# Optimization experiments

Measured on AMD Instinct MI355X. Metric: run time of the kernel, lower is better.

Reference implementation:

```python
import jax, jax.numpy as jnp
import numpy as np

HIDDEN = 4096
NUM_HEADS = 32
NUM_KV_HEADS = 8
HEAD_DIM = 128
EPS = 1e-6
ROPE_THETA = 1000000.0
T = 2048


def setup_inputs() -> dict:
    key = jax.random.key(0)
    k1, k2, k3, k4, k5 = jax.random.split(key, 5)
    q_size = NUM_HEADS * HEAD_DIM
    kv_size = NUM_KV_HEADS * HEAD_DIM
    return {
        "positions": jnp.arange(T, dtype=jnp.int32),
        "hidden_states": jax.random.normal(k1, (T, HIDDEN), dtype=jnp.float32),
        "w_qkv": jax.random.normal(k2, (HIDDEN, q_size + 2 * kv_size), dtype=jnp.float32) * 0.02,
        "w_o": jax.random.normal(k3, (q_size, HIDDEN), dtype=jnp.float32) * 0.02,
        "q_norm_w": jnp.ones((HEAD_DIM,), dtype=jnp.float32) + 0.01 * jax.random.normal(k4, (HEAD_DIM,), dtype=jnp.float32),
        "k_norm_w": jnp.ones((HEAD_DIM,), dtype=jnp.float32) + 0.01 * jax.random.normal(k5, (HEAD_DIM,), dtype=jnp.float32),
    }


def _rms_norm(x, w, eps=EPS):
    # x: [..., head_dim], normalize over last dim
    var = jnp.mean(jnp.square(x), axis=-1, keepdims=True)
    return x * jax.lax.rsqrt(var + eps) * w


def _apply_rope(x, positions):
    # neox-style rotate-half RoPE, rotary_dim == head_dim
    d = x.shape[-1]
    inv_freq = 1.0 / (ROPE_THETA ** (jnp.arange(0, d, 2, dtype=jnp.float32) / d))
    freqs = positions.astype(jnp.float32)[:, None] * inv_freq[None, :]  # [T, d/2]
    cos = jnp.cos(freqs)[:, None, :]  # [T, 1, d/2]
    sin = jnp.sin(freqs)[:, None, :]
    x1, x2 = jnp.split(x, 2, axis=-1)
    return jnp.concatenate([x1 * cos - x2 * sin, x2 * cos + x1 * sin], axis=-1)


def reference(positions, hidden_states, w_qkv, w_o, q_norm_w, k_norm_w):
    num_tokens = hidden_states.shape[0]
    q_size = NUM_HEADS * HEAD_DIM
    kv_size = NUM_KV_HEADS * HEAD_DIM
    group = NUM_HEADS // NUM_KV_HEADS

    qkv = hidden_states @ w_qkv  # [T, q+2kv]
    q = qkv[:, :q_size].reshape(num_tokens, NUM_HEADS, HEAD_DIM)
    k = qkv[:, q_size:q_size + kv_size].reshape(num_tokens, NUM_KV_HEADS, HEAD_DIM)
    v = qkv[:, q_size + kv_size:].reshape(num_tokens, NUM_KV_HEADS, HEAD_DIM)

    q = _rms_norm(q, q_norm_w)
    k = _rms_norm(k, k_norm_w)
    q = _apply_rope(q, positions)
    k = _apply_rope(k, positions)

    scale = HEAD_DIM ** -0.5
    # GQA: group query heads over shared kv heads
    qg = q.reshape(num_tokens, NUM_KV_HEADS, group, HEAD_DIM)
    scores = jnp.einsum("tkgd,skd->kgts", qg * scale, k)  # [KH, G, T, S]
    causal = positions[:, None] >= positions[None, :]  # [T, S]
    scores = jnp.where(causal[None, None, :, :], scores, jnp.finfo(scores.dtype).min)
    probs = jax.nn.softmax(scores, axis=-1)
    out = jnp.einsum("kgts,skd->tkgd", probs, v)  # [T, KH, G, D]
    out = out.reshape(num_tokens, q_size)
    return out @ w_o
```

## Files before the change

### kernel.cpp

```cpp
#include <hip/hip_runtime.h>
#include <cstdint>
#include <cstddef>

#define T_TOK 2048
#define HID   4096
#define NQH   32
#define NKVH  8
#define HD    128
#define QKV_N 6144

typedef __bf16 bf16x8 __attribute__((ext_vector_type(8)));
typedef __bf16 bf16x4 __attribute__((ext_vector_type(4)));
typedef float  f32x4  __attribute__((ext_vector_type(4)));
typedef float  f32x16 __attribute__((ext_vector_type(16)));

#define AS1 __attribute__((address_space(1)))
#define AS3 __attribute__((address_space(3)))

__device__ __forceinline__ void gll16(const void* g, void* l) {
  __builtin_amdgcn_global_load_lds((const AS1 void*)g, (AS3 void*)l, 16, 0, 0);
}

__global__ __launch_bounds__(256) void k_convert(const float* __restrict__ in,
                                                 __bf16* __restrict__ out, int n4) {
  int i = blockIdx.x * 256 + threadIdx.x;
  if (i >= n4) return;
  float4 v = ((const float4*)in)[i];
  bf16x4 o;
  o[0] = (__bf16)v.x; o[1] = (__bf16)v.y; o[2] = (__bf16)v.z; o[3] = (__bf16)v.w;
  ((bf16x4*)out)[i] = o;
}

__global__ __launch_bounds__(256) void k_transpose(const float* __restrict__ in,
                                                   __bf16* __restrict__ out,
                                                   int R, int C) {
  __shared__ float tile[64][65];
  const int tid = threadIdx.x;
  const int c0 = blockIdx.x * 64, r0 = blockIdx.y * 64;
  const int ty = tid >> 4, tx = tid & 15;
#pragma unroll
  for (int k = 0; k < 4; ++k) {
    float4 v = *(const float4*)&in[(size_t)(r0 + ty + k * 16) * C + c0 + tx * 4];
    tile[ty + k * 16][tx * 4 + 0] = v.x;
    tile[ty + k * 16][tx * 4 + 1] = v.y;
    tile[ty + k * 16][tx * 4 + 2] = v.z;
    tile[ty + k * 16][tx * 4 + 3] = v.w;
  }
  __syncthreads();
  const int c = tid >> 2, rq = tid & 3;
#pragma unroll
  for (int h = 0; h < 2; ++h) {
    bf16x8 o;
#pragma unroll
    for (int i = 0; i < 8; ++i) o[i] = (__bf16)tile[rq * 16 + h * 8 + i][c];
    *(bf16x8*)&out[(size_t)(c0 + c) * R + r0 + rq * 16 + h * 8] = o;
  }
}

template <int NFR, typename OUT>
__global__ __launch_bounds__(512, 2) void k_gemm8(const __bf16* __restrict__ A,
                                                  const __bf16* __restrict__ Bt,
                                                  OUT* __restrict__ C,
                                                  int N, int K) {
  constexpr int BN   = 64 * NFR;
  constexpr int WN   = 16 * NFR;
  constexpr int NB   = NFR / 2;
  constexpr int NH   = NFR / 2;
  constexpr int BREG = BN * 64;
  constexpr int BUFSZ = 16384 + 2 * BREG;
  __shared__ alignas(16) char ldsb[2 * BUFSZ];
  const int tid = threadIdx.x;
  const int lane = tid & 63, w = tid >> 6;
  const int l16 = lane & 15, lg = lane >> 4;
  const int wm = w >> 2, wn = w & 3;

  const int x = blockIdx.x & 7, idx = blockIdx.x >> 3;
  const int bm = (x & 1) * 8 + (idx & 7);
  const int bn = (x >> 1) * 4 + (idx >> 3);

  const int rA = tid >> 2, pA = tid & 3;
  const __bf16* asrc = A + (size_t)(bm * 128 + rA) * K + ((pA ^ ((rA >> 1) & 3)) * 8);
  const __bf16* bsrc = Bt + (size_t)(bn * BN + rA) * K + ((pA ^ ((rA >> 1) & 3)) * 8);

#define RA_(buf, mk) (ldsb + (buf) * BUFSZ + (mk) * 8192)
#define RB_(buf, mk) (ldsb + (buf) * BUFSZ + 16384 + (mk) * BREG)
#define STG_A(buf, mk, kk) { gll16(asrc + (kk) + (mk) * 32, RA_(buf, mk) + w * 1024); }
#define STG_B(buf, mk, kk) { _Pragma("unroll") \
    for (int j = 0; j < NB; ++j) \
      gll16(bsrc + (size_t)j * 128 * K + (kk) + (mk) * 32, RB_(buf, mk) + j * 8192 + w * 1024); }
#define FRAG(base, row) (*(const bf16x8*)((base) + (row) * 64 + ((lg ^ (((row) >> 1) & 3)) << 4)))
#define WAITN() { if constexpr (NFR == 6) asm volatile("s_waitcnt vmcnt(4)" ::: "memory"); \
                  else                    asm volatile("s_waitcnt vmcnt(3)" ::: "memory"); }

  f32x4 acc[4][NFR] = {};
  const int nkt = K >> 6;

  STG_A(0, 0, 0); STG_B(0, 0, 0); STG_A(0, 1, 0); STG_B(0, 1, 0);

  for (int t = 0; t < nkt - 1; ++t) {
    const int cur = t & 1, nxt = cur ^ 1;
    const int kn = (t + 1) * 64;
    bf16x8 af[4], bf_[NH];

    STG_A(nxt, 0, kn);
    WAITN();
    __builtin_amdgcn_s_barrier();
    __builtin_amdgcn_sched_barrier(0);
#pragma unroll
    for (int i = 0; i < 4; ++i) af[i] = FRAG(RA_(cur, 0), wm * 64 + i * 16 + l16);
#pragma unroll
    for (int n = 0; n < NH; ++n) bf_[n] = FRAG(RB_(cur, 0), wn * WN + n * 16 + l16);
    __builtin_amdgcn_s_setprio(1);
#pragma unroll
    for (int i = 0; i < 4; ++i)
#pragma unroll
      for (int n = 0; n < NH; ++n)
        acc[i][n] = __builtin_amdgcn_mfma_f32_16x16x32_bf16(af[i], bf_[n], acc[i][n], 0, 0, 0);
    __builtin_amdgcn_s_setprio(0);
    __builtin_amdgcn_s_barrier();

#pragma unroll
    for (int n = 0; n < NH; ++n) bf_[n] = FRAG(RB_(cur, 0), wn * WN + (NH + n) * 16 + l16);
    STG_B(nxt, 0, kn);
    __builtin_amdgcn_s_barrier();
    __builtin_amdgcn_s_setprio(1);
#pragma unroll
    for (int i = 0; i < 4; ++i)
#pragma unroll
      for (int n = 0; n < NH; ++n)
        acc[i][NH + n] = __builtin_amdgcn_mfma_f32_16x16x32_bf16(af[i], bf_[n], acc[i][NH + n], 0, 0, 0);
    __builtin_amdgcn_s_setprio(0);
    __builtin_amdgcn_s_barrier();

    STG_A(nxt, 1, kn);
    WAITN();
    __builtin_amdgcn_s_barrier();
    __builtin_amdgcn_sched_barrier(0);
#pragma unroll
    for (int i = 0; i < 4; ++i) af[i] = FRAG(RA_(cur, 1), wm * 64 + i * 16 + l16);
#pragma unroll
    for (int n = 0; n < NH; ++n) bf_[n] = FRAG(RB_(cur, 1), wn * WN + n * 16 + l16);
    __builtin_amdgcn_s_setprio(1);
#pragma unroll
    for (int i = 0; i < 4; ++i)
#pragma unroll
      for (int n = 0; n < NH; ++n)
        acc[i][n] = __builtin_amdgcn_mfma_f32_16x16x32_bf16(af[i], bf_[n], acc[i][n], 0, 0, 0);
    __builtin_amdgcn_s_setprio(0);
    __builtin_amdgcn_s_barrier();

#pragma unroll
    for (int n = 0; n < NH; ++n) bf_[n] = FRAG(RB_(cur, 1), wn * WN + (NH + n) * 16 + l16);
    STG_B(nxt, 1, kn);
    __builtin_amdgcn_s_barrier();
    __builtin_amdgcn_s_setprio(1);
#pragma unroll
    for (int i = 0; i < 4; ++i)
#pragma unroll
      for (int n = 0; n < NH; ++n)
        acc[i][NH + n] = __builtin_amdgcn_mfma_f32_16x16x32_bf16(af[i], bf_[n], acc[i][NH + n], 0, 0, 0);
    __builtin_amdgcn_s_setprio(0);
    __builtin_amdgcn_s_barrier();
  }

  asm volatile("s_waitcnt vmcnt(0)" ::: "memory");
  __builtin_amdgcn_s_barrier();
  __builtin_amdgcn_sched_barrier(0);
  {
    const int cur = (nkt - 1) & 1;
#pragma unroll
    for (int mk = 0; mk < 2; ++mk) {
      bf16x8 aa[4], bb[NFR];
#pragma unroll
      for (int i = 0; i < 4; ++i) aa[i] = FRAG(RA_(cur, mk), wm * 64 + i * 16 + l16);
#pragma unroll
      for (int n = 0; n < NFR; ++n) bb[n] = FRAG(RB_(cur, mk), wn * WN + n * 16 + l16);
#pragma unroll
      for (int i = 0; i < 4; ++i)
#pragma unroll
        for (int n = 0; n < NFR; ++n)
          acc[i][n] = __builtin_amdgcn_mfma_f32_16x16x32_bf16(aa[i], bb[n], acc[i][n], 0, 0, 0);
    }
  }
#undef RA_
#undef RB_
#undef STG_A
#undef STG_B
#undef FRAG
#undef WAITN

#pragma unroll
  for (int mi = 0; mi < 4; ++mi)
#pragma unroll
    for (int ni = 0; ni < NFR; ++ni) {
      int row = bm * 128 + wm * 64 + mi * 16 + lg * 4;
      int col = bn * BN + wn * WN + ni * 16 + l16;
#pragma unroll
      for (int r = 0; r < 4; ++r)
        C[(size_t)(row + r) * N + col] = (OUT)acc[mi][ni][r];
    }
}

__global__ __launch_bounds__(256) void k_norm_rope(const __bf16* __restrict__ qkv,
                                                   const int* __restrict__ pos,
                                                   const float* __restrict__ qw,
                                                   const float* __restrict__ kw,
                                                   __bf16* __restrict__ qo,
                                                   __bf16* __restrict__ ko,
                                                   __bf16* __restrict__ vto) {
  __shared__ float tile[64][65];
  const int tid = threadIdx.x;
  if (blockIdx.x >= T_TOK) {
    const int tb = blockIdx.x - T_TOK;
    const int d0 = (tb & 1) * 64;
    const int t0 = ((tb >> 1) & 31) * 64;
    const int kvh = tb >> 6;
    const int ty = tid >> 4, tx = tid & 15;
#pragma unroll
    for (int k = 0; k < 4; ++k) {
      bf16x4 v = *(const bf16x4*)&qkv[(size_t)(t0 + ty + k * 16) * QKV_N + 5120 + kvh * 128 + d0 + tx * 4];
#pragma unroll
      for (int j = 0; j < 4; ++j) tile[ty + k * 16][tx * 4 + j] = (float)v[j];
    }
    __syncthreads();
    const int d = tid >> 2, tq = tid & 3;
#pragma unroll
    for (int h = 0; h < 2; ++h) {
      bf16x8 o;
#pragma unroll
      for (int i = 0; i < 8; ++i) o[i] = (__bf16)tile[tq * 16 + h * 8 + i][d];
      *(bf16x8*)&vto[((size_t)kvh * 128 + d0 + d) * T_TOK + t0 + tq * 16 + h * 8] = o;
    }
    return;
  }
  const int t = blockIdx.x;
  const int w = tid >> 6, i = tid & 63;
  const float fr = (float)pos[t] * expf((float)i * -0.21586735246819178f);
  const float cs = cosf(fr), sn = sinf(fr);
  const float qwi1 = qw[i], qwi2 = qw[i + 64];
  const float kwi1 = kw[i], kwi2 = kw[i + 64];
  const __bf16* base = qkv + (size_t)t * QKV_N;
#pragma unroll
  for (int s = 0; s < 10; ++s) {
    const int slot = w * 10 + s;
    const int off = (slot < 32) ? slot * 128 : 4096 + (slot - 32) * 128;
    float x1 = (float)base[off + i], x2 = (float)base[off + i + 64];
    float ss = x1 * x1 + x2 * x2;
#pragma unroll
    for (int m = 32; m >= 1; m >>= 1) ss += __shfl_xor(ss, m);
    float rinv = rsqrtf(ss * (1.0f / 128.0f) + 1e-6f);
    float n1, n2;
    if (slot < 32) { n1 = x1 * rinv * qwi1; n2 = x2 * rinv * qwi2; }
    else           { n1 = x1 * rinv * kwi1; n2 = x2 * rinv * kwi2; }
    float o1 = n1 * cs - n2 * sn;
    float o2 = n2 * cs + n1 * sn;
    if (slot < 32) {
      const float QSC = 0.08838834764831845f * 1.4426950408889634f;
      __bf16* o = qo + ((size_t)t * NQH + slot) * HD;
      o[i] = (__bf16)(o1 * QSC);
      o[i + 64] = (__bf16)(o2 * QSC);
    } else {
      __bf16* o = ko + ((size_t)t * NKVH + (slot - 32)) * HD;
      o[i] = (__bf16)o1;
      o[i + 64] = (__bf16)o2;
    }
  }
}

__global__ __launch_bounds__(256, 2) void k_attn(const __bf16* __restrict__ Q,
                                                 const __bf16* __restrict__ K,
                                                 const __bf16* __restrict__ Vt,
                                                 __bf16* __restrict__ O,
                                                 const float* __restrict__ wo,
                                                 __bf16* __restrict__ wot) {
  __shared__ alignas(16) char lds[32768];
  const int tid = threadIdx.x;
  if (blockIdx.x >= 512) {
    const int tb = blockIdx.x - 512;
    const int c0 = (tb & 63) * 64, r0 = (tb >> 6) * 64;
    float (*tile)[65] = (float(*)[65])lds;
    const int ty = tid >> 4, tx = tid & 15;
#pragma unroll
    for (int k = 0; k < 4; ++k) {
      float4 v = *(const float4*)&wo[(size_t)(r0 + ty + k * 16) * HID + c0 + tx * 4];
      tile[ty + k * 16][tx * 4 + 0] = v.x;
      tile[ty + k * 16][tx * 4 + 1] = v.y;
      tile[ty + k * 16][tx * 4 + 2] = v.z;
      tile[ty + k * 16][tx * 4 + 3] = v.w;
    }
    __syncthreads();
    const int c = tid >> 2, rq = tid & 3;
#pragma unroll
    for (int h = 0; h < 2; ++h) {
      bf16x8 o;
#pragma unroll
      for (int i = 0; i < 8; ++i) o[i] = (__bf16)tile[rq * 16 + h * 8 + i][c];
      *(bf16x8*)&wot[(size_t)(c0 + c) * HID + r0 + rq * 16 + h * 8] = o;
    }
    return;
  }
  const int bid = blockIdx.x;
  const int kvh = bid & 7;
  const int raw = bid >> 3;
  const int qc  = (raw < 32) ? 63 - raw : raw - 32;
  const int lane = tid & 63, w = tid >> 6;
  const int l31 = lane & 31, hi = lane >> 5;
  const int h  = kvh * 4 + w;
  const int q0 = qc * 32;
  const int qrow = q0 + l31;
  char* Ksb = lds;
  char* Vtb = lds + 16384;

  bf16x8 qf[8];
  {
    const __bf16* qp = Q + ((size_t)qrow * NQH + h) * HD + hi * 8;
#pragma unroll
    for (int dc = 0; dc < 8; ++dc)
      qf[dc] = *(const bf16x8*)(qp + dc * 16);
  }

  size_t ksrc[4], vsrc[4];
#pragma unroll
  for (int j = 0; j < 4; ++j) {
    int kr = w * 16 + j * 4 + (lane >> 4);
    ksrc[j] = ((size_t)kr * NKVH + kvh) * HD + (size_t)(((lane & 15) ^ (kr & 15)) * 8);
    int vr = w * 32 + j * 8 + (lane >> 3);
    vsrc[j] = ((size_t)(kvh * HD + vr)) * T_TOK + (size_t)(((lane & 7) ^ (vr & 7)) * 8);
  }

  float m_run = -3.0e38f, l_run = 0.f;
  f32x16 ot[4] = {};

  const int ntiles = (qc >> 1) + 1;
  for (int tt = 0; tt < ntiles; ++tt) {
    const int s0 = tt * 64;
#pragma unroll
    for (int j = 0; j < 4; ++j) {
      gll16(K + (size_t)s0 * (NKVH * HD) + ksrc[j], Ksb + (w * 4 + j) * 1024);
      gll16(Vt + (size_t)s0 + vsrc[j], Vtb + (w * 4 + j) * 1024);
    }
    __syncthreads();

    f32x16 sac[2] = {};
#pragma unroll
    for (int hf = 0; hf < 2; ++hf) {
      int krow = hf * 32 + l31;
#pragma unroll
      for (int dc = 0; dc < 8; ++dc) {
        bf16x8 kf = *(const bf16x8*)(Ksb + krow * 256 + (((dc * 2 + hi) ^ (krow & 15)) * 16));
        sac[hf] = __builtin_amdgcn_mfma_f32_32x32x16_bf16(kf, qf[dc], sac[hf], 0, 0, 0);
      }
    }

    float pv[32];
    if (s0 + 64 > q0) {
#pragma unroll
      for (int hf = 0; hf < 2; ++hf)
#pragma unroll
        for (int r = 0; r < 16; ++r) {
          int kvg = s0 + hf * 32 + (r & 3) + ((r >> 2) * 8) + hi * 4;
          pv[hf * 16 + r] = (kvg > qrow) ? -3.0e38f : sac[hf][r];
        }
    } else {
#pragma unroll
      for (int hf = 0; hf < 2; ++hf)
#pragma unroll
        for (int r = 0; r < 16; ++r) pv[hf * 16 + r] = sac[hf][r];
    }
    float t16[16];
#pragma unroll
    for (int i = 0; i < 16; ++i) t16[i] = fmaxf(pv[i], pv[i + 16]);
#pragma unroll
    for (int i = 0; i < 8; ++i) t16[i] = fmaxf(t16[i], t16[i + 8]);
#pragma unroll
    for (int i = 0; i < 4; ++i) t16[i] = fmaxf(t16[i], t16[i + 4]);
    float mt = fmaxf(fmaxf(t16[0], t16[1]), fmaxf(t16[2], t16[3]));
    mt = fmaxf(mt, __shfl_xor(mt, 32));
    if (!__all(mt - m_run <= 10.0f)) {
      float m_new = fmaxf(m_run, mt);
      float corr = exp2f(m_run - m_new);
      l_run *= corr;
#pragma unroll
      for (int dt = 0; dt < 4; ++dt)
#pragma unroll
        for (int r = 0; r < 16; ++r) ot[dt][r] *= corr;
      m_run = m_new;
    }
#pragma unroll
    for (int i = 0; i < 32; ++i) pv[i] = exp2f(pv[i] - m_run);
#pragma unroll
    for (int i = 0; i < 16; ++i) t16[i] = pv[i] + pv[i + 16];
#pragma unroll
    for (int i = 0; i < 8; ++i) t16[i] += t16[i + 8];
#pragma unroll
    for (int i = 0; i < 4; ++i) t16[i] += t16[i + 4];
    float rs = (t16[0] + t16[1]) + (t16[2] + t16[3]);
    rs += __shfl_xor(rs, 32);
    l_run += rs;

    uint32_t wds[16];
#pragma unroll
    for (int i = 0; i < 16; ++i) {
      uint32_t r;
      asm("v_cvt_pk_bf16_f32 %0, %1, %2" : "=v"(r) : "v"(pv[2 * i]), "v"(pv[2 * i + 1]));
      wds[i] = r;
    }
#pragma unroll
    for (int c = 0; c < 4; ++c) {
      const int base = (c >> 1) * 8 + (c & 1) * 4;
      uint32_t sa = hi ? wds[base + 0] : wds[base + 2];
      uint32_t sb = hi ? wds[base + 1] : wds[base + 3];
      uint32_t ra = __shfl_xor(sa, 32);
      uint32_t rb = __shfl_xor(sb, 32);
      union { uint32_t u[4]; bf16x8 v; } pf;
      pf.u[0] = hi ? ra : wds[base + 0];
      pf.u[1] = hi ? rb : wds[base + 1];
      pf.u[2] = hi ? wds[base + 2] : ra;
      pf.u[3] = hi ? wds[base + 3] : rb;
#pragma unroll
      for (int dt = 0; dt < 4; ++dt) {
        int vrow = dt * 32 + l31;
        bf16x8 vf = *(const bf16x8*)(Vtb + vrow * 128 + (((c * 2 + hi) ^ (vrow & 7)) * 16));
        ot[dt] = __builtin_amdgcn_mfma_f32_32x32x16_bf16(vf, pf.v, ot[dt], 0, 0, 0);
      }
    }
    __syncthreads();
  }

  float inv = 1.0f / l_run;
  char* Ob = Ksb + w * 8192;
#pragma unroll
  for (int dt = 0; dt < 4; ++dt)
#pragma unroll
    for (int r = 0; r < 16; ++r) {
      int d = dt * 32 + (r & 3) + ((r >> 2) * 8) + hi * 4;
      *(__bf16*)(Ob + l31 * 256 + ((d * 2) ^ ((l31 & 7) << 4))) = (__bf16)(ot[dt][r] * inv);
    }
  __builtin_amdgcn_s_barrier();
#pragma unroll
  for (int pass = 0; pass < 8; ++pass) {
    int q = pass * 4 + (lane >> 4);
    int ch = lane & 15;
    bf16x8 vvv = *(const bf16x8*)(Ob + q * 256 + ((ch ^ (q & 7)) * 16));
    *(bf16x8*)(O + ((size_t)(q0 + q) * NQH + h) * HD + ch * 8) = vvv;
  }
}

extern "C" void kernel_launch(void* const* d_in, const int* in_sizes, int n_in,
                              void* d_out, int out_size, void* d_ws, size_t ws_size,
                              hipStream_t stream) {
  const int*   positions = (const int*)d_in[0];
  const float* hidden    = (const float*)d_in[1];
  const float* w_qkv     = (const float*)d_in[2];
  const float* w_o       = (const float*)d_in[3];
  const float* q_norm    = (const float*)d_in[4];
  const float* k_norm    = (const float*)d_in[5];
  float* out = (float*)d_out;

  char* ws = (char*)d_ws;
  __bf16* wqkv_t   = (__bf16*)ws;
  __bf16* wo_t     = (__bf16*)(ws + 50331648);
  __bf16* hidden_b = (__bf16*)(ws + 83886080);
  __bf16* qkvb     = (__bf16*)(ws + 100663296);
  __bf16* qb  = (__bf16*)ws;
  __bf16* kb  = (__bf16*)(ws + 16777216);
  __bf16* vtb = (__bf16*)(ws + 20971520);
  __bf16* attn_o = hidden_b;

  k_convert<<<dim3((T_TOK * HID / 4 + 255) / 256), 256, 0, stream>>>(hidden, hidden_b, T_TOK * HID / 4);
  k_transpose<<<dim3(QKV_N / 64, HID / 64), 256, 0, stream>>>(w_qkv, wqkv_t, HID, QKV_N);
  k_gemm8<6, __bf16><<<dim3(256), 512, 0, stream>>>(hidden_b, wqkv_t, qkvb, QKV_N, HID);
  k_norm_rope<<<dim3(T_TOK + 512), 256, 0, stream>>>(qkvb, positions, q_norm, k_norm, qb, kb, vtb);
  k_attn<<<dim3(512 + 4096), 256, 0, stream>>>(qb, kb, vtb, attn_o, w_o, wo_t);
  k_gemm8<4, float><<<dim3(256), 512, 0, stream>>>(attn_o, wo_t, out, HID, HID);
}
```

Measured before the change: 295.7 us.

## Fuse QK norm/RoPE/V-transpose into QKV GEMM epilogue and merge prep kernels

Merges the hidden-state bf16 conversion and the w_qkv transpose into a single launch. It also moves the per-head RMSNorm, RoPE and V transpose into the QKV GEMM epilogue. The epilogue stages the output tile in LDS, so the intermediate qkv buffer is never written to or read back from global memory. The cost is a heavier, serial epilogue: each wave handles 16 rows with shuffle reductions and uncoalesced scalar bf16 stores. The V transpose writes only 2-byte elements.

Result: no change. 300.9 us (+1.8%).

```diff
diff --git a/kernel.cpp b/kernel.cpp
--- a/kernel.cpp
+++ b/kernel.cpp
@@ -21,26 +21,26 @@
   __builtin_amdgcn_global_load_lds((const AS1 void*)g, (AS3 void*)l, 16, 0, 0);
 }
 
-__global__ __launch_bounds__(256) void k_convert(const float* __restrict__ in,
-                                                 __bf16* __restrict__ out, int n4) {
-  int i = blockIdx.x * 256 + threadIdx.x;
-  if (i >= n4) return;
-  float4 v = ((const float4*)in)[i];
-  bf16x4 o;
-  o[0] = (__bf16)v.x; o[1] = (__bf16)v.y; o[2] = (__bf16)v.z; o[3] = (__bf16)v.w;
-  ((bf16x4*)out)[i] = o;
-}
-
-__global__ __launch_bounds__(256) void k_transpose(const float* __restrict__ in,
-                                                   __bf16* __restrict__ out,
-                                                   int R, int C) {
+__global__ __launch_bounds__(256) void k_prep(const float* __restrict__ hidden,
+                                              __bf16* __restrict__ hidden_b,
+                                              const float* __restrict__ wqkv,
+                                              __bf16* __restrict__ wqkv_t) {
   __shared__ float tile[64][65];
   const int tid = threadIdx.x;
-  const int c0 = blockIdx.x * 64, r0 = blockIdx.y * 64;
+  if (blockIdx.x < 8192) {
+    int i = blockIdx.x * 256 + tid;
+    float4 v = ((const float4*)hidden)[i];
+    bf16x4 o;
+    o[0] = (__bf16)v.x; o[1] = (__bf16)v.y; o[2] = (__bf16)v.z; o[3] = (__bf16)v.w;
+    ((bf16x4*)hidden_b)[i] = o;
+    return;
+  }
+  const int tb = blockIdx.x - 8192;
+  const int c0 = (tb % 96) * 64, r0 = (tb / 96) * 64;
   const int ty = tid >> 4, tx = tid & 15;
 #pragma unroll
   for (int k = 0; k < 4; ++k) {
-    float4 v = *(const float4*)&in[(size_t)(r0 + ty + k * 16) * C + c0 + tx * 4];
+    float4 v = *(const float4*)&wqkv[(size_t)(r0 + ty + k * 16) * QKV_N + c0 + tx * 4];
     tile[ty + k * 16][tx * 4 + 0] = v.x;
     tile[ty + k * 16][tx * 4 + 1] = v.y;
     tile[ty + k * 16][tx * 4 + 2] = v.z;
@@ -53,15 +53,21 @@
     bf16x8 o;
 #pragma unroll
     for (int i = 0; i < 8; ++i) o[i] = (__bf16)tile[rq * 16 + h * 8 + i][c];
-    *(bf16x8*)&out[(size_t)(c0 + c) * R + r0 + rq * 16 + h * 8] = o;
+    *(bf16x8*)&wqkv_t[(size_t)(c0 + c) * HID + r0 + rq * 16 + h * 8] = o;
   }
 }
 
-template <int NFR, typename OUT>
+template <int NFR, typename OUT, bool NORM>
 __global__ __launch_bounds__(512, 2) void k_gemm8(const __bf16* __restrict__ A,
                                                   const __bf16* __restrict__ Bt,
                                                   OUT* __restrict__ C,
-                                                  int N, int K) {
+                                                  int N, int K,
+                                                  const int* __restrict__ pos,
+                                                  const float* __restrict__ qw,
+                                                  const float* __restrict__ kw,
+                                                  __bf16* __restrict__ qo,
+                                                  __bf16* __restrict__ ko,
+                                                  __bf16* __restrict__ vto) {
   constexpr int BN   = 64 * NFR;
   constexpr int WN   = 16 * NFR;
   constexpr int NB   = NFR / 2;
@@ -189,80 +195,77 @@
 #undef FRAG
 #undef WAITN
 
-#pragma unroll
-  for (int mi = 0; mi < 4; ++mi)
-#pragma unroll
-    for (int ni = 0; ni < NFR; ++ni) {
-      int row = bm * 128 + wm * 64 + mi * 16 + lg * 4;
-      int col = bn * BN + wn * WN + ni * 16 + l16;
-#pragma unroll
-      for (int r = 0; r < 4; ++r)
-        C[(size_t)(row + r) * N + col] = (OUT)acc[mi][ni][r];
-    }
-}
-
-__global__ __launch_bounds__(256) void k_norm_rope(const __bf16* __restrict__ qkv,
-                                                   const int* __restrict__ pos,
-                                                   const float* __restrict__ qw,
-                                                   const float* __restrict__ kw,
-                                                   __bf16* __restrict__ qo,
-                                                   __bf16* __restrict__ ko,
-                                                   __bf16* __restrict__ vto) {
-  __shared__ float tile[64][65];
-  const int tid = threadIdx.x;
-  if (blockIdx.x >= T_TOK) {
-    const int tb = blockIdx.x - T_TOK;
-    const int d0 = (tb & 1) * 64;
-    const int t0 = ((tb >> 1) & 31) * 64;
-    const int kvh = tb >> 6;
-    const int ty = tid >> 4, tx = tid & 15;
-#pragma unroll
-    for (int k = 0; k < 4; ++k) {
-      bf16x4 v = *(const bf16x4*)&qkv[(size_t)(t0 + ty + k * 16) * QKV_N + 5120 + kvh * 128 + d0 + tx * 4];
-#pragma unroll
-      for (int j = 0; j < 4; ++j) tile[ty + k * 16][tx * 4 + j] = (float)v[j];
-    }
+  if constexpr (!NORM) {
+#pragma unroll
+    for (int mi = 0; mi < 4; ++mi)
+#pragma unroll
+      for (int ni = 0; ni < NFR; ++ni) {
+        int row = bm * 128 + wm * 64 + mi * 16 + lg * 4;
+        int col = bn * BN + wn * WN + ni * 16 + l16;
+#pragma unroll
+        for (int r = 0; r < 4; ++r)
+          C[(size_t)(row + r) * N + col] = (OUT)acc[mi][ni][r];
+      }
+  } else {
     __syncthreads();
-    const int d = tid >> 2, tq = tid & 3;
-#pragma unroll
-    for (int h = 0; h < 2; ++h) {
-      bf16x8 o;
-#pragma unroll
-      for (int i = 0; i < 8; ++i) o[i] = (__bf16)tile[tq * 16 + h * 8 + i][d];
-      *(bf16x8*)&vto[((size_t)kvh * 128 + d0 + d) * T_TOK + t0 + tq * 16 + h * 8] = o;
-    }
-    return;
-  }
-  const int t = blockIdx.x;
-  const int w = tid >> 6, i = tid & 63;
-  const float fr = (float)pos[t] * expf((float)i * -0.21586735246819178f);
-  const float cs = cosf(fr), sn = sinf(fr);
-  const float qwi1 = qw[i], qwi2 = qw[i + 64];
-  const float kwi1 = kw[i], kwi2 = kw[i + 64];
-  const __bf16* base = qkv + (size_t)t * QKV_N;
-#pragma unroll
-  for (int s = 0; s < 10; ++s) {
-    const int slot = w * 10 + s;
-    const int off = (slot < 32) ? slot * 128 : 4096 + (slot - 32) * 128;
-    float x1 = (float)base[off + i], x2 = (float)base[off + i + 64];
-    float ss = x1 * x1 + x2 * x2;
-#pragma unroll
-    for (int m = 32; m >= 1; m >>= 1) ss += __shfl_xor(ss, m);
-    float rinv = rsqrtf(ss * (1.0f / 128.0f) + 1e-6f);
-    float n1, n2;
-    if (slot < 32) { n1 = x1 * rinv * qwi1; n2 = x2 * rinv * qwi2; }
-    else           { n1 = x1 * rinv * kwi1; n2 = x2 * rinv * kwi2; }
-    float o1 = n1 * cs - n2 * sn;
-    float o2 = n2 * cs + n1 * sn;
-    if (slot < 32) {
-      const float QSC = 0.08838834764831845f * 1.4426950408889634f;
-      __bf16* o = qo + ((size_t)t * NQH + slot) * HD;
-      o[i] = (__bf16)(o1 * QSC);
-      o[i + 64] = (__bf16)(o2 * QSC);
-    } else {
-      __bf16* o = ko + ((size_t)t * NKVH + (slot - 32)) * HD;
-      o[i] = (__bf16)o1;
-      o[i + 64] = (__bf16)o2;
+    __bf16 (*tile)[394] = (__bf16(*)[394])ldsb;
+#pragma unroll
+    for (int mi = 0; mi < 4; ++mi)
+#pragma unroll
+      for (int ni = 0; ni < NFR; ++ni) {
+        int row = wm * 64 + mi * 16 + lg * 4;
+        int col = wn * WN + ni * 16 + l16;
+#pragma unroll
+        for (int r = 0; r < 4; ++r)
+          tile[row + r][col] = (__bf16)acc[mi][ni][r];
+      }
+    __syncthreads();
+    const float qw1 = qw[lane], qw2 = qw[lane + 64];
+    const float kw1 = kw[lane], kw2 = kw[lane + 64];
+    const float iexp = expf((float)lane * -0.21586735246819178f);
+    for (int tr = 0; tr < 16; ++tr) {
+      const int trow = w * 16 + tr;
+      const int tok = bm * 128 + trow;
+      const float fr = (float)pos[tok] * iexp;
+      const float cs = cosf(fr), sn = sinf(fr);
+#pragma unroll
+      for (int hh = 0; hh < 3; ++hh) {
+        const int hid = bn * 3 + hh;
+        if (hid >= 40) continue;
+        float x1 = (float)tile[trow][hh * 128 + lane];
+        float x2 = (float)tile[trow][hh * 128 + 64 + lane];
+        float ss = x1 * x1 + x2 * x2;
+#pragma unroll
+        for (int m = 32; m >= 1; m >>= 1) ss += __shfl_xor(ss, m);
+        float rinv = rsqrtf(ss * (1.0f / 128.0f) + 1e-6f);
+        float n1, n2;
+        if (hid < 32) { n1 = x1 * rinv * qw1; n2 = x2 * rinv * qw2; }
+        else          { n1 = x1 * rinv * kw1; n2 = x2 * rinv * kw2; }
+        float o1 = n1 * cs - n2 * sn;
+        float o2 = n2 * cs + n1 * sn;
+        if (hid < 32) {
+          const float QSC = 0.08838834764831845f * 1.4426950408889634f;
+          __bf16* o = qo + ((size_t)tok * NQH + hid) * HD;
+          o[lane] = (__bf16)(o1 * QSC);
+          o[lane + 64] = (__bf16)(o2 * QSC);
+        } else {
+          __bf16* o = ko + ((size_t)tok * NKVH + (hid - 32)) * HD;
+          o[lane] = (__bf16)o1;
+          o[lane + 64] = (__bf16)o2;
+        }
+      }
+    }
+#pragma unroll
+    for (int hh = 0; hh < 3; ++hh) {
+      const int hid = bn * 3 + hh;
+      if (hid < 40) continue;
+      const int kvh = hid - 40;
+      const int tkn = tid & 127, dq = tid >> 7;
+#pragma unroll
+      for (int dp = 0; dp < 32; ++dp) {
+        int d = dp * 4 + dq;
+        vto[((size_t)(kvh * 128 + d)) * T_TOK + bm * 128 + tkn] = tile[tkn][hh * 128 + d];
+      }
     }
   }
 }
@@ -461,16 +464,15 @@
   __bf16* wqkv_t   = (__bf16*)ws;
   __bf16* wo_t     = (__bf16*)(ws + 50331648);
   __bf16* hidden_b = (__bf16*)(ws + 83886080);
-  __bf16* qkvb     = (__bf16*)(ws + 100663296);
-  __bf16* qb  = (__bf16*)ws;
-  __bf16* kb  = (__bf16*)(ws + 16777216);
-  __bf16* vtb = (__bf16*)(ws + 20971520);
+  __bf16* qb  = (__bf16*)(ws + 100663296);
+  __bf16* kb  = (__bf16*)(ws + 117440512);
+  __bf16* vtb = (__bf16*)(ws + 121634816);
   __bf16* attn_o = hidden_b;
 
-  k_convert<<<dim3((T_TOK * HID / 4 + 255) / 256), 256, 0, stream>>>(hidden, hidden_b, T_TOK * HID / 4);
-  k_transpose<<<dim3(QKV_N / 64, HID / 64), 256, 0, stream>>>(w_qkv, wqkv_t, HID, QKV_N);
-  k_gemm8<6, __bf16><<<dim3(256), 512, 0, stream>>>(hidden_b, wqkv_t, qkvb, QKV_N, HID);
-  k_norm_rope<<<dim3(T_TOK + 512), 256, 0, stream>>>(qkvb, positions, q_norm, k_norm, qb, kb, vtb);
+  k_prep<<<dim3(8192 + 6144), 256, 0, stream>>>(hidden, hidden_b, w_qkv, wqkv_t);
+  k_gemm8<6, __bf16, true><<<dim3(256), 512, 0, stream>>>(
+      hidden_b, wqkv_t, nullptr, QKV_N, HID, positions, q_norm, k_norm, qb, kb, vtb);
   k_attn<<<dim3(512 + 4096), 256, 0, stream>>>(qb, kb, vtb, attn_o, w_o, wo_t);
-  k_gemm8<4, float><<<dim3(256), 512, 0, stream>>>(attn_o, wo_t, out, HID, HID);
+  k_gemm8<4, float, false><<<dim3(256), 512, 0, stream>>>(
+      attn_o, wo_t, out, HID, HID, nullptr, nullptr, nullptr, nullptr, nullptr, nullptr);
 }
```
